# Optimization experiments

Measured on AMD Instinct MI355X. Metric: run time of the kernel, lower is better.

The kernel has to match this reference:

```python
import jax, jax.numpy as jnp
import numpy as np

B, D, N, M, R, C = 512, 16, 64, 32, 32, 10  # batch, divisions, feat_in, feat_map, TR-rank, categories


def setup_inputs() -> dict:
    key = jax.random.key(0)
    k1, k2, k3, k4 = jax.random.split(key, 4)
    tensor = jax.random.normal(k1, (B, D, N), dtype=jnp.float32)
    W_fm = jax.random.normal(k2, (N, M), dtype=jnp.float32) / np.sqrt(N)
    b_fm = jax.random.normal(k3, (M,), dtype=jnp.float32) * 0.01
    # one [R, M, R] tensor-ring core per (category, division)
    G = jax.random.normal(k4, (C, D, R, M, R), dtype=jnp.float32) / np.sqrt(M * R)
    return {"tensor": tensor, "W_fm": W_fm, "b_fm": b_fm, "G": G}


def reference(tensor, W_fm, b_fm, G):
    # FeatureMap: learned linear n -> m applied per division  [B, D, M]
    feat = jnp.einsum('bdn,nm->bdm', tensor, W_fm) + b_fm
    # CoreKernelTensorRing per (category, division): [B,M] x [R,M,R] -> [B,R,R]
    cores = jnp.einsum('bdm,cdimj->cdbij', feat, G)  # [C, D, B, R, R]
    # __foward_products: chained batched matmul along divisions (structural loop, D fixed)
    prod = cores[:, 0]  # [C, B, R, R]
    for d in range(1, D):
        prod = jnp.matmul(prod, cores[:, d])
    # __calculate_traces: per-sample trace, one logit per category
    logits = jnp.einsum('cbii->bc', prod)  # [B, C]
    return jax.nn.log_softmax(logits, axis=1)
```

## Files before the change

### kernel.cpp

```cpp
#include <hip/hip_runtime.h>
#include <math.h>

#define BB 512
#define DD 16
#define NN 64
#define MM 32
#define RR 32
#define CC 10
#define BBLK 16
#define SETS 2
#define ROWH 40
#define BREGH 1304

typedef _Float16 v8h __attribute__((ext_vector_type(8)));
typedef float v4f __attribute__((ext_vector_type(4)));

union H8 { unsigned int u[4]; v8h h; _Float16 e[8]; };
union H4 { unsigned int u[2]; _Float16 e[4]; };

__global__ __launch_bounds__(256) void produce_kernel(
    const float* __restrict__ tensor, const float* __restrict__ W,
    const float* __restrict__ bias,   const float* __restrict__ G,
    _Float16* __restrict__ fh,        _Float16* __restrict__ gh) {
    __shared__ __align__(16) char smem[36864];
    const int t = threadIdx.x;
    if (blockIdx.x < 1024) {
        float* ten_s = (float*)smem;
        float* W_s   = (float*)smem + 512;
        const int bd0 = blockIdx.x * 8;
        if (t < 128)
            *(float4*)(ten_s + t * 4) = *(const float4*)(tensor + bd0 * NN + t * 4);
        *(float4*)(W_s + t * 4)        = *(const float4*)(W + t * 4);
        *(float4*)(W_s + 1024 + t * 4) = *(const float4*)(W + 1024 + t * 4);
        __syncthreads();
        const int m = t & 31, bd_l = t >> 5;
        float acc = bias[m];
#pragma unroll
        for (int n = 0; n < NN; ++n) acc += ten_s[bd_l * NN + n] * W_s[n * MM + m];
        fh[(bd0 + bd_l) * MM + m] = (_Float16)acc;
    } else {
        _Float16* lg = (_Float16*)smem;
        const int pb = blockIdx.x - 1024;
        const int c  = pb >> 5;
        const int d  = (pb >> 1) & 15;
        const int hf = pb & 1;
        const float* src = G + (size_t)(c * DD + d) * 32768 + hf * 16384;
#pragma unroll
        for (int k = 0; k < 16; ++k) {
            const int f = (k * 256 + t) * 4;
            float4 v = *(const float4*)(src + f);
            const int di = f >> 10, m = (f >> 5) & 31, j = f & 31;
            H4 hv;
            hv.e[0] = (_Float16)v.x; hv.e[1] = (_Float16)v.y;
            hv.e[2] = (_Float16)v.z; hv.e[3] = (_Float16)v.w;
            *(uint2*)(lg + di * 1152 + m * 36 + j) = make_uint2(hv.u[0], hv.u[1]);
        }
        __syncthreads();
#pragma unroll
        for (int k = 0; k < 8; ++k) {
            const int idx = k * 256 + t;
            const int tl = idx >> 6, ln = idx & 63;
            const int di = tl >> 1, jh = tl & 1;
            const int q = ln >> 4, j4 = ln & 15;
            const int j = jh * 16 + j4;
            H8 o;
#pragma unroll
            for (int r = 0; r < 8; ++r)
                o.e[r] = lg[di * 1152 + (8 * q + r) * 36 + j];
            const size_t gi = ((size_t)(c * DD + d) * 64 + hf * 32 + tl) * 64 + ln;
            *(v8h*)(gh + gi * 8) = o.h;
        }
    }
}

__global__ __launch_bounds__(512, 2) void chain_kernel(
    const _Float16* __restrict__ feat_h,
    const _Float16* __restrict__ g_h,
    float* __restrict__ trout)
{
    __shared__ __align__(16) _Float16 lds[SETS * BBLK * BREGH];

    const int bid = blockIdx.x;
    const int xcd = bid & 7;
    const int idx = bid >> 3;
    int c, sub;
    if (idx < 16) { c = xcd; sub = idx; }
    else {
        const int e = idx - 16;
        c = 8 + (xcd >> 2);
        sub = (xcd & 3) * 4 + e;
    }
    const int b0 = sub * (SETS * BBLK);
    const int t    = threadIdx.x;
    const int w    = t >> 6;
    const int lane = t & 63;
    const int q    = lane >> 4;
    const int j4   = lane & 15;

    const size_t gc = (size_t)c * DD * 32768;

    v8h afh[2];
#pragma unroll
    for (int bs = 0; bs < 2; ++bs)
        afh[bs] = *(const v8h*)(feat_h + (size_t)(b0 + 16 * bs + j4) * (DD * MM) + q * 8);
    v8h gf[8];
#pragma unroll
    for (int u = 0; u < 8; ++u)
        gf[u] = *(const v8h*)(g_h + gc + ((size_t)(w * 8 + u) * 64 + lane) * 8);

    v8h sb[4][2];

    for (int d = 0; d < DD; ++d) {
        __syncthreads();
        v4f av[2][8];
#pragma unroll
        for (int bs = 0; bs < 2; ++bs)
#pragma unroll
            for (int u = 0; u < 8; ++u) {
                v4f z = {0.f, 0.f, 0.f, 0.f};
                av[bs][u] = __builtin_amdgcn_mfma_f32_16x16x32_f16(
                    afh[bs], gf[u], z, 0, 0, 0);
            }
        if (d < DD - 1) {
#pragma unroll
            for (int bs = 0; bs < 2; ++bs)
                afh[bs] = *(const v8h*)(feat_h +
                    (size_t)(b0 + 16 * bs + j4) * (DD * MM) + (d + 1) * MM + q * 8);
            const size_t gb = gc + (size_t)(d + 1) * 32768;
#pragma unroll
            for (int u = 0; u < 8; ++u)
                gf[u] = *(const v8h*)(g_h + gb + ((size_t)(w * 8 + u) * 64 + lane) * 8);
        }
#pragma unroll
        for (int bs = 0; bs < 2; ++bs)
#pragma unroll
            for (int jh = 0; jh < 2; ++jh)
#pragma unroll
                for (int reg = 0; reg < 4; ++reg) {
                    H4 hv;
                    hv.e[0] = (_Float16)av[bs][0 + jh][reg];
                    hv.e[1] = (_Float16)av[bs][2 + jh][reg];
                    hv.e[2] = (_Float16)av[bs][4 + jh][reg];
                    hv.e[3] = (_Float16)av[bs][6 + jh][reg];
                    *(uint2*)(&lds[(bs * BBLK + 4 * q + reg) * BREGH +
                                   (16 * jh + j4) * ROWH + 4 * w]) =
                        make_uint2(hv.u[0], hv.u[1]);
                }
        __syncthreads();
#pragma unroll
        for (int ch = 0; ch < 4; ++ch) {
            const int bs = ch >> 1;
            const int bl = 2 * w + (ch & 1);
            _Float16* base = lds + (bs * BBLK + bl) * BREGH;
            if (d == 0) {
#pragma unroll
                for (int vt = 0; vt < 2; ++vt) {
                    H8 x;
#pragma unroll
                    for (int r = 0; r < 8; ++r)
                        x.e[r] = base[(8 * q + r) * ROWH + 16 * vt + j4];
                    sb[ch][vt] = x.h;
                }
            } else {
                v8h af2[2];
#pragma unroll
                for (int jt = 0; jt < 2; ++jt)
                    af2[jt] = *(const v8h*)(base + (16 * jt + j4) * ROWH + 8 * q);
                if (d == DD - 1) {
                    v4f z0 = {0.f, 0.f, 0.f, 0.f};
                    v4f a0 = __builtin_amdgcn_mfma_f32_16x16x32_f16(
                        af2[0], sb[ch][0], z0, 0, 0, 0);
                    v4f z1 = {0.f, 0.f, 0.f, 0.f};
                    v4f a1 = __builtin_amdgcn_mfma_f32_16x16x32_f16(
                        af2[1], sb[ch][1], z1, 0, 0, 0);
                    float ts = 0.f;
#pragma unroll
                    for (int reg = 0; reg < 4; ++reg)
                        if (j4 == 4 * q + reg) ts = a0[reg] + a1[reg];
#pragma unroll
                    for (int off = 32; off > 0; off >>= 1)
                        ts += __shfl_xor(ts, off);
                    if (lane == 0)
                        trout[(size_t)(b0 + 16 * bs + bl) * CC + c] = ts;
                } else {
                    v4f acc[2][2];
#pragma unroll
                    for (int jt = 0; jt < 2; ++jt)
#pragma unroll
                        for (int vt = 0; vt < 2; ++vt) {
                            v4f z = {0.f, 0.f, 0.f, 0.f};
                            acc[jt][vt] = __builtin_amdgcn_mfma_f32_16x16x32_f16(
                                af2[jt], sb[ch][vt], z, 0, 0, 0);
                        }
#pragma unroll
                    for (int jt = 0; jt < 2; ++jt)
#pragma unroll
                        for (int vt = 0; vt < 2; ++vt) {
                            H4 hv;
                            hv.e[0] = (_Float16)acc[jt][vt][0];
                            hv.e[1] = (_Float16)acc[jt][vt][1];
                            hv.e[2] = (_Float16)acc[jt][vt][2];
                            hv.e[3] = (_Float16)acc[jt][vt][3];
                            *(uint2*)(base + (16 * vt + j4) * ROWH + 16 * jt + 4 * q) =
                                make_uint2(hv.u[0], hv.u[1]);
                        }
                    __builtin_amdgcn_sched_barrier(0);
#pragma unroll
                    for (int vt = 0; vt < 2; ++vt)
                        sb[ch][vt] = *(const v8h*)(base + (16 * vt + j4) * ROWH + 8 * q);
                }
            }
        }
    }
}

__global__ __launch_bounds__(256) void lsm_kernel(
    const float* __restrict__ tr, float* __restrict__ out) {
    const int b = blockIdx.x * 256 + threadIdx.x;
    float v[CC];
    float mx = -1e30f;
#pragma unroll
    for (int c = 0; c < CC; ++c) {
        v[c] = tr[b * CC + c];
        mx = fmaxf(mx, v[c]);
    }
    float ssum = 0.f;
#pragma unroll
    for (int c = 0; c < CC; ++c) ssum += expf(v[c] - mx);
    const float ls = logf(ssum);
#pragma unroll
    for (int c = 0; c < CC; ++c) out[b * CC + c] = v[c] - mx - ls;
}

extern "C" void kernel_launch(void* const* d_in, const int* in_sizes, int n_in,
                              void* d_out, int out_size, void* d_ws, size_t ws_size,
                              hipStream_t stream) {
    const float* tensor = (const float*)d_in[0];
    const float* W      = (const float*)d_in[1];
    const float* bias   = (const float*)d_in[2];
    const float* G      = (const float*)d_in[3];
    float* out = (float*)d_out;

    const size_t FEAT = (size_t)BB * DD * MM;
    const size_t GPK  = (size_t)CC * DD * 64 * 64 * 8;
    _Float16* fh = (_Float16*)d_ws;
    _Float16* gh = fh + FEAT;
    float* trbuf = (float*)(gh + GPK);

    produce_kernel<<<1024 + 320, 256, 0, stream>>>(tensor, W, bias, G, fh, gh);
    chain_kernel<<<CC * (BB / (SETS * BBLK)), 512, 0, stream>>>(fh, gh, trbuf);
    lsm_kernel<<<BB / 256, 256, 0, stream>>>(trbuf, out);
}
```

Baseline: 117.0 us.

## Switch chain kernel to 32x32x16 MFMA and keep running product in registers

Rewrites the chain kernel to use 32x32x16 f16 MFMA tiles instead of 16x16x32, which changes how the packed G operand is laid out in the produce kernel. Each wave now handles four whole samples with one 32x32 product per sample. The running product is moved into the next B operand with lane shuffles rather than a store to and reload from LDS, which removes that per-step LDS traffic. In exchange the kernel does extra shuffle and select work, and register pressure rises because of the 16-wide accumulators.

```diff
diff --git a/kernel.cpp b/kernel.cpp
--- a/kernel.cpp
+++ b/kernel.cpp
@@ -7,16 +7,21 @@
 #define MM 32
 #define RR 32
 #define CC 10
-#define BBLK 16
-#define SETS 2
-#define ROWH 40
-#define BREGH 1304
+#define ISTR 40
+#define BSTR 1288
 
 typedef _Float16 v8h __attribute__((ext_vector_type(8)));
 typedef float v4f __attribute__((ext_vector_type(4)));
+typedef float v16f __attribute__((ext_vector_type(16)));
 
 union H8 { unsigned int u[4]; v8h h; _Float16 e[8]; };
 union H4 { unsigned int u[2]; _Float16 e[4]; };
+
+__device__ inline unsigned pk2(float a, float b) {
+    union { unsigned u; _Float16 e[2]; } v;
+    v.e[0] = (_Float16)a; v.e[1] = (_Float16)b;
+    return v.u;
+}
 
 __global__ __launch_bounds__(256) void produce_kernel(
     const float* __restrict__ tensor, const float* __restrict__ W,
@@ -60,13 +65,12 @@
         for (int k = 0; k < 8; ++k) {
             const int idx = k * 256 + t;
             const int tl = idx >> 6, ln = idx & 63;
-            const int di = tl >> 1, jh = tl & 1;
-            const int q = ln >> 4, j4 = ln & 15;
-            const int j = jh * 16 + j4;
+            const int di = tl >> 1, ks = tl & 1;
+            const int hh = ln >> 5, j = ln & 31;
             H8 o;
 #pragma unroll
             for (int r = 0; r < 8; ++r)
-                o.e[r] = lg[di * 1152 + (8 * q + r) * 36 + j];
+                o.e[r] = lg[di * 1152 + (16 * ks + 8 * hh + r) * 36 + j];
             const size_t gi = ((size_t)(c * DD + d) * 64 + hf * 32 + tl) * 64 + ln;
             *(v8h*)(gh + gi * 8) = o.h;
         }
@@ -78,7 +82,7 @@
     const _Float16* __restrict__ g_h,
     float* __restrict__ trout)
 {
-    __shared__ __align__(16) _Float16 lds[SETS * BBLK * BREGH];
+    __shared__ __align__(16) _Float16 lds[32 * BSTR];
 
     const int bid = blockIdx.x;
     const int xcd = bid & 7;
@@ -90,124 +94,119 @@
         c = 8 + (xcd >> 2);
         sub = (xcd & 3) * 4 + e;
     }
-    const int b0 = sub * (SETS * BBLK);
+    const int b0 = sub * 32;
     const int t    = threadIdx.x;
     const int w    = t >> 6;
     const int lane = t & 63;
-    const int q    = lane >> 4;
-    const int j4   = lane & 15;
+    const int h    = lane >> 5;
+    const int col  = lane & 31;
 
     const size_t gc = (size_t)c * DD * 32768;
-
-    v8h afh[2];
-#pragma unroll
-    for (int bs = 0; bs < 2; ++bs)
-        afh[bs] = *(const v8h*)(feat_h + (size_t)(b0 + 16 * bs + j4) * (DD * MM) + q * 8);
-    v8h gf[8];
-#pragma unroll
-    for (int u = 0; u < 8; ++u)
-        gf[u] = *(const v8h*)(g_h + gc + ((size_t)(w * 8 + u) * 64 + lane) * 8);
+    const _Float16* fb = feat_h + (size_t)(b0 + col) * (DD * MM);
+
+    const v16f z16 = {0.f,0.f,0.f,0.f,0.f,0.f,0.f,0.f,
+                      0.f,0.f,0.f,0.f,0.f,0.f,0.f,0.f};
+
+    v8h af[2];
+#pragma unroll
+    for (int ks = 0; ks < 2; ++ks)
+        af[ks] = *(const v8h*)(fb + 16 * ks + 8 * h);
+    v8h gB[4][2];
+#pragma unroll
+    for (int il = 0; il < 4; ++il)
+#pragma unroll
+        for (int ks = 0; ks < 2; ++ks)
+            gB[il][ks] = *(const v8h*)(g_h + gc +
+                ((size_t)(((4 * w + il) * 2 + ks) * 64) + lane) * 8);
 
     v8h sb[4][2];
 
     for (int d = 0; d < DD; ++d) {
         __syncthreads();
-        v4f av[2][8];
-#pragma unroll
-        for (int bs = 0; bs < 2; ++bs)
-#pragma unroll
-            for (int u = 0; u < 8; ++u) {
-                v4f z = {0.f, 0.f, 0.f, 0.f};
-                av[bs][u] = __builtin_amdgcn_mfma_f32_16x16x32_f16(
-                    afh[bs], gf[u], z, 0, 0, 0);
-            }
+        v16f av[4];
+#pragma unroll
+        for (int il = 0; il < 4; ++il) {
+            av[il] = __builtin_amdgcn_mfma_f32_32x32x16_f16(af[0], gB[il][0], z16, 0, 0, 0);
+            av[il] = __builtin_amdgcn_mfma_f32_32x32x16_f16(af[1], gB[il][1], av[il], 0, 0, 0);
+        }
         if (d < DD - 1) {
 #pragma unroll
-            for (int bs = 0; bs < 2; ++bs)
-                afh[bs] = *(const v8h*)(feat_h +
-                    (size_t)(b0 + 16 * bs + j4) * (DD * MM) + (d + 1) * MM + q * 8);
+            for (int ks = 0; ks < 2; ++ks)
+                af[ks] = *(const v8h*)(fb + (d + 1) * MM + 16 * ks + 8 * h);
             const size_t gb = gc + (size_t)(d + 1) * 32768;
 #pragma unroll
-            for (int u = 0; u < 8; ++u)
-                gf[u] = *(const v8h*)(g_h + gb + ((size_t)(w * 8 + u) * 64 + lane) * 8);
-        }
-#pragma unroll
-        for (int bs = 0; bs < 2; ++bs)
-#pragma unroll
-            for (int jh = 0; jh < 2; ++jh)
-#pragma unroll
-                for (int reg = 0; reg < 4; ++reg) {
-                    H4 hv;
-                    hv.e[0] = (_Float16)av[bs][0 + jh][reg];
-                    hv.e[1] = (_Float16)av[bs][2 + jh][reg];
-                    hv.e[2] = (_Float16)av[bs][4 + jh][reg];
-                    hv.e[3] = (_Float16)av[bs][6 + jh][reg];
-                    *(uint2*)(&lds[(bs * BBLK + 4 * q + reg) * BREGH +
-                                   (16 * jh + j4) * ROWH + 4 * w]) =
-                        make_uint2(hv.u[0], hv.u[1]);
-                }
-        __syncthreads();
-#pragma unroll
-        for (int ch = 0; ch < 4; ++ch) {
-            const int bs = ch >> 1;
-            const int bl = 2 * w + (ch & 1);
-            _Float16* base = lds + (bs * BBLK + bl) * BREGH;
+            for (int il = 0; il < 4; ++il)
+#pragma unroll
+                for (int ks = 0; ks < 2; ++ks)
+                    gB[il][ks] = *(const v8h*)(g_h + gb +
+                        ((size_t)(((4 * w + il) * 2 + ks) * 64) + lane) * 8);
+        }
+#pragma unroll
+        for (int r16 = 0; r16 < 16; ++r16) {
+            const int b = (r16 & 3) + 8 * (r16 >> 2) + 4 * h;
+            H4 hv;
+            hv.e[0] = (_Float16)av[0][r16];
+            hv.e[1] = (_Float16)av[1][r16];
+            hv.e[2] = (_Float16)av[2][r16];
+            hv.e[3] = (_Float16)av[3][r16];
+            *(uint2*)(lds + b * BSTR + col * ISTR + 4 * w) =
+                make_uint2(hv.u[0], hv.u[1]);
+        }
+        __syncthreads();
+#pragma unroll
+        for (int cc = 0; cc < 4; ++cc) {
+            _Float16* base = lds + (4 * w + cc) * BSTR;
             if (d == 0) {
 #pragma unroll
-                for (int vt = 0; vt < 2; ++vt) {
+                for (int ks = 0; ks < 2; ++ks) {
                     H8 x;
 #pragma unroll
                     for (int r = 0; r < 8; ++r)
-                        x.e[r] = base[(8 * q + r) * ROWH + 16 * vt + j4];
-                    sb[ch][vt] = x.h;
+                        x.e[r] = base[(16 * ks + 8 * h + r) * ISTR + col];
+                    sb[cc][ks] = x.h;
                 }
             } else {
-                v8h af2[2];
-#pragma unroll
-                for (int jt = 0; jt < 2; ++jt)
-                    af2[jt] = *(const v8h*)(base + (16 * jt + j4) * ROWH + 8 * q);
+                v8h a0 = *(const v8h*)(base + col * ISTR + 8 * h);
+                v8h a1 = *(const v8h*)(base + col * ISTR + 16 + 8 * h);
+                v16f acc;
+                acc = __builtin_amdgcn_mfma_f32_32x32x16_f16(a0, sb[cc][0], z16, 0, 0, 0);
+                acc = __builtin_amdgcn_mfma_f32_32x32x16_f16(a1, sb[cc][1], acc, 0, 0, 0);
                 if (d == DD - 1) {
-                    v4f z0 = {0.f, 0.f, 0.f, 0.f};
-                    v4f a0 = __builtin_amdgcn_mfma_f32_16x16x32_f16(
-                        af2[0], sb[ch][0], z0, 0, 0, 0);
-                    v4f z1 = {0.f, 0.f, 0.f, 0.f};
-                    v4f a1 = __builtin_amdgcn_mfma_f32_16x16x32_f16(
-                        af2[1], sb[ch][1], z1, 0, 0, 0);
                     float ts = 0.f;
 #pragma unroll
-                    for (int reg = 0; reg < 4; ++reg)
-                        if (j4 == 4 * q + reg) ts = a0[reg] + a1[reg];
+                    for (int r16 = 0; r16 < 16; ++r16) {
+                        const int row = (r16 & 3) + 8 * (r16 >> 2) + 4 * h;
+                        if (row == col) ts += acc[r16];
+                    }
 #pragma unroll
                     for (int off = 32; off > 0; off >>= 1)
                         ts += __shfl_xor(ts, off);
                     if (lane == 0)
-                        trout[(size_t)(b0 + 16 * bs + bl) * CC + c] = ts;
+                        trout[(size_t)(b0 + 4 * w + cc) * CC + c] = ts;
                 } else {
-                    v4f acc[2][2];
-#pragma unroll
-                    for (int jt = 0; jt < 2; ++jt)
-#pragma unroll
-                        for (int vt = 0; vt < 2; ++vt) {
-                            v4f z = {0.f, 0.f, 0.f, 0.f};
-                            acc[jt][vt] = __builtin_amdgcn_mfma_f32_16x16x32_f16(
-                                af2[jt], sb[ch][vt], z, 0, 0, 0);
-                        }
-#pragma unroll
-                    for (int jt = 0; jt < 2; ++jt)
-#pragma unroll
-                        for (int vt = 0; vt < 2; ++vt) {
-                            H4 hv;
-                            hv.e[0] = (_Float16)acc[jt][vt][0];
-                            hv.e[1] = (_Float16)acc[jt][vt][1];
-                            hv.e[2] = (_Float16)acc[jt][vt][2];
-                            hv.e[3] = (_Float16)acc[jt][vt][3];
-                            *(uint2*)(base + (16 * vt + j4) * ROWH + 16 * jt + 4 * q) =
-                                make_uint2(hv.u[0], hv.u[1]);
-                        }
-                    __builtin_amdgcn_sched_barrier(0);
-#pragma unroll
-                    for (int vt = 0; vt < 2; ++vt)
-                        sb[ch][vt] = *(const v8h*)(base + (16 * vt + j4) * ROWH + 8 * q);
+                    const unsigned A0 = pk2(acc[0],  acc[1]);
+                    const unsigned A1 = pk2(acc[2],  acc[3]);
+                    const unsigned B0 = pk2(acc[4],  acc[5]);
+                    const unsigned B1 = pk2(acc[6],  acc[7]);
+                    const unsigned C0 = pk2(acc[8],  acc[9]);
+                    const unsigned C1 = pk2(acc[10], acc[11]);
+                    const unsigned D0 = pk2(acc[12], acc[13]);
+                    const unsigned D1 = pk2(acc[14], acc[15]);
+                    const unsigned pA0 = (unsigned)__shfl_xor((int)A0, 32);
+                    const unsigned pA1 = (unsigned)__shfl_xor((int)A1, 32);
+                    const unsigned pB0 = (unsigned)__shfl_xor((int)B0, 32);
+                    const unsigned pB1 = (unsigned)__shfl_xor((int)B1, 32);
+                    const unsigned pC0 = (unsigned)__shfl_xor((int)C0, 32);
+                    const unsigned pC1 = (unsigned)__shfl_xor((int)C1, 32);
+                    const unsigned pD0 = (unsigned)__shfl_xor((int)D0, 32);
+                    const unsigned pD1 = (unsigned)__shfl_xor((int)D1, 32);
+                    H8 s0, s1;
+                    s0.u[0] = h ? pB0 : A0;  s0.u[1] = h ? pB1 : A1;
+                    s0.u[2] = h ? B0 : pA0;  s0.u[3] = h ? B1 : pA1;
+                    s1.u[0] = h ? pD0 : C0;  s1.u[1] = h ? pD1 : C1;
+                    s1.u[2] = h ? D0 : pC0;  s1.u[3] = h ? D1 : pC1;
+                    sb[cc][0] = s0.h;
+                    sb[cc][1] = s1.h;
                 }
             }
         }
@@ -248,6 +247,6 @@
     float* trbuf = (float*)(gh + GPK);
 
     produce_kernel<<<1024 + 320, 256, 0, stream>>>(tensor, W, bias, G, fh, gh);
-    chain_kernel<<<CC * (BB / (SETS * BBLK)), 512, 0, stream>>>(fh, gh, trbuf);
+    chain_kernel<<<160, 512, 0, stream>>>(fh, gh, trbuf);
     lsm_kernel<<<BB / 256, 256, 0, stream>>>(trbuf, out);
 }
```

Result: slower. 120.4 us (+2.9%).
